# Kernel optimization log

Measured on AMD Instinct MI355X. Metric: run time of the kernel, lower is better.

The kernel has to match this reference:

```python
import jax, jax.numpy as jnp
import numpy as np

B = 64        # decode batch (num_tokens)
S = 2048      # max_kv_len
H = 2048      # hidden_size
HQ = 16       # num query heads
HKV = 4       # num kv heads
D = 128       # head_dim
RD = 64       # rope_dim = head_dim * 0.5
P = B * S     # kv pool size
EPS = 1e-6
SCALE = D ** -0.5


def rms_norm(x, w):
    xf = x.astype(jnp.float32)
    var = jnp.mean(xf * xf, axis=-1, keepdims=True)
    return (w.astype(jnp.float32) * (xf * jax.lax.rsqrt(var + EPS))).astype(x.dtype)


def rotate_half(x):
    x1, x2 = x[..., : x.shape[-1] // 2], x[..., x.shape[-1] // 2:]
    return jnp.concatenate([-x2, x1], axis=-1)


def apply_rope(x, cos, sin):
    # x: [T, heads, D]; cos/sin: [T, 1, RD]; partial rotary on first RD dims
    x_rot, x_pass = x[..., :RD], x[..., RD:]
    x_emb = x_rot * cos + rotate_half(x_rot) * sin
    return jnp.concatenate([x_emb, x_pass], axis=-1)


def setup_inputs() -> dict:
    key = jax.random.key(0)
    ks = jax.random.split(key, 10)
    f32 = jnp.float32
    hidden_states = jax.random.normal(ks[0], (B, H), f32)
    Wq = jax.random.normal(ks[1], (HQ * D, H), f32) * 0.02
    Wk = jax.random.normal(ks[2], (HKV * D, H), f32) * 0.02
    Wv = jax.random.normal(ks[3], (HKV * D, H), f32) * 0.02
    Wo = jax.random.normal(ks[4], (H, HQ * D), f32) * 0.02
    q_norm_w = jnp.ones((D,), f32)
    k_norm_w = jnp.ones((D,), f32)
    key_cache = jax.random.normal(ks[5], (P, HKV, D), f32)
    value_cache = jax.random.normal(ks[6], (P, HKV, D), f32)
    seq_lens = jax.random.randint(ks[7], (B,), S // 2, S + 1).astype(jnp.int32)
    req_pool_indices = jnp.arange(B, dtype=jnp.int32)
    req_to_token = jnp.arange(P, dtype=jnp.int32).reshape(B, S)
    out_cache_loc = (req_pool_indices * S + (seq_lens - 1)).astype(jnp.int32)
    # RoPE tables for the current decode positions (seq_len - 1)
    pos = (seq_lens - 1).astype(f32)
    inv_freq = 1.0 / (10000.0 ** (jnp.arange(0, RD, 2, dtype=f32) / RD))  # [RD/2]
    ang = pos[:, None] * inv_freq[None, :]                                 # [B, RD/2]
    cos = jnp.concatenate([jnp.cos(ang), jnp.cos(ang)], axis=-1)           # [B, RD]
    sin = jnp.concatenate([jnp.sin(ang), jnp.sin(ang)], axis=-1)
    return dict(hidden_states=hidden_states, Wq=Wq, Wk=Wk, Wv=Wv,
                q_norm_w=q_norm_w, k_norm_w=k_norm_w, Wo=Wo,
                key_cache=key_cache, value_cache=value_cache, cos=cos, sin=sin,
                req_to_token=req_to_token, req_pool_indices=req_pool_indices,
                seq_lens=seq_lens, out_cache_loc=out_cache_loc)


def reference(hidden_states, Wq, Wk, Wv, q_norm_w, k_norm_w, Wo,
              key_cache, value_cache, cos, sin,
              req_to_token, req_pool_indices, seq_lens, out_cache_loc):
    G = HQ // HKV  # GQA groups
    # fused qkv projection
    q = (hidden_states @ Wq.T).reshape(B, HQ, D)
    k = (hidden_states @ Wk.T).reshape(B, HKV, D)
    v = (hidden_states @ Wv.T).reshape(B, HKV, D)
    # per-head RMSNorm
    q = rms_norm(q, q_norm_w)
    k = rms_norm(k, k_norm_w)
    # partial rotary embedding (sliding_attention layer -> rope applied)
    q = apply_rope(q, cos[:, None, :], sin[:, None, :])
    k = apply_rope(k, cos[:, None, :], sin[:, None, :])
    # write new token K/V into the paged pool
    key_cache = key_cache.at[out_cache_loc].set(k)
    value_cache = value_cache.at[out_cache_loc].set(v)
    # paged gather: [B, S, HKV, D]
    token_indices = req_to_token[req_pool_indices]
    k_pad = key_cache[token_indices].transpose(0, 2, 1, 3)    # [B, HKV, S, D]
    v_pad = value_cache[token_indices].transpose(0, 2, 1, 3)  # [B, HKV, S, D]
    # padding mask over kv positions
    mask = jnp.arange(S)[None, :] < seq_lens[:, None]          # [B, S]
    # attention (q_len = 1 per request), grouped-query
    qg = q.reshape(B, HKV, G, D)
    scores = jnp.einsum('bkgd,bksd->bkgs', qg, k_pad) * SCALE  # [B, HKV, G, S]
    scores = jnp.where(mask[:, None, None, :], scores, jnp.finfo(scores.dtype).min)
    attn = jax.nn.softmax(scores, axis=-1)
    out = jnp.einsum('bkgs,bksd->bkgd', attn, v_pad).reshape(B, HQ * D)
    return out @ Wo.T
```

## Files before the change

kernel.cpp:

```cpp
#include <hip/hip_runtime.h>
#include <math.h>

#define BB 64
#define SS 2048
#define HH 2048
#define HQ 16
#define HKV 4
#define DD 128
#define RD 64
#define GG 4
#define QKV_N 3072
#define SCALE 0.08838834764831845f
#define KSPLIT 16
#define KRANGE (HH / KSPLIT)
#define NSPLIT 8
#define CHUNK 256

__device__ __forceinline__ void gemm_tile(const float* __restrict__ A,
                                          const float* __restrict__ W,
                                          float* __restrict__ Cpart,
                                          int ldC, int colbase, int wrow0, int ks) {
  __shared__ __align__(16) float As[32][68];
  __shared__ __align__(16) float Ws[32][132];
  const int tid = threadIdx.x;
  const int tm = tid >> 4, tn = tid & 15;
  float acc[4][8] = {};
  const int k0 = ks * KRANGE;
  for (int kk = k0; kk < k0 + KRANGE; kk += 32) {
    #pragma unroll
    for (int p = tid; p < 512; p += 256) {
      const int mm = p >> 3, cc = p & 7;
      const float4 a = *(const float4*)(A + (size_t)mm * HH + kk + cc * 4);
      As[cc*4+0][mm] = a.x; As[cc*4+1][mm] = a.y;
      As[cc*4+2][mm] = a.z; As[cc*4+3][mm] = a.w;
    }
    #pragma unroll
    for (int p = tid; p < 1024; p += 256) {
      const int rr = p >> 3, cc = p & 7;
      const float4 w = *(const float4*)(W + (size_t)(wrow0 + rr) * HH + kk + cc * 4);
      Ws[cc*4+0][rr] = w.x; Ws[cc*4+1][rr] = w.y;
      Ws[cc*4+2][rr] = w.z; Ws[cc*4+3][rr] = w.w;
    }
    __syncthreads();
    #pragma unroll
    for (int k = 0; k < 32; k++) {
      const float4 av  = *(const float4*)&As[k][tm * 4];
      const float4 wv0 = *(const float4*)&Ws[k][tn * 8];
      const float4 wv1 = *(const float4*)&Ws[k][tn * 8 + 4];
      const float a4[4] = {av.x, av.y, av.z, av.w};
      const float w8[8] = {wv0.x, wv0.y, wv0.z, wv0.w, wv1.x, wv1.y, wv1.z, wv1.w};
      #pragma unroll
      for (int i = 0; i < 4; i++)
        #pragma unroll
        for (int j = 0; j < 8; j++)
          acc[i][j] += a4[i] * w8[j];
    }
    __syncthreads();
  }
  #pragma unroll
  for (int i = 0; i < 4; i++) {
    float* dst = Cpart + (size_t)(tm*4 + i) * ldC + colbase + tn*8;
    *(float4*)dst       = make_float4(acc[i][0], acc[i][1], acc[i][2], acc[i][3]);
    *(float4*)(dst + 4) = make_float4(acc[i][4], acc[i][5], acc[i][6], acc[i][7]);
  }
}

__global__ __launch_bounds__(256) void maple_gemm_qkv(const float* __restrict__ A,
                                                      const float* __restrict__ Wq,
                                                      const float* __restrict__ Wk,
                                                      const float* __restrict__ Wv,
                                                      float* __restrict__ qkv_part) {
  const int col0 = blockIdx.x * 128;
  const int ks = blockIdx.y;
  const float* W; int wrow0;
  if (col0 < 2048)      { W = Wq; wrow0 = col0; }
  else if (col0 < 2560) { W = Wk; wrow0 = col0 - 2048; }
  else                  { W = Wv; wrow0 = col0 - 2560; }
  gemm_tile(A, W, qkv_part + (size_t)ks * BB * QKV_N, QKV_N, col0, wrow0, ks);
}

__global__ __launch_bounds__(256) void maple_gemm_o(const float* __restrict__ A,
                                                    const float* __restrict__ W,
                                                    float* __restrict__ out_part) {
  const int col0 = blockIdx.x * 128;
  const int ks = blockIdx.y;
  gemm_tile(A, W, out_part + (size_t)ks * BB * HH, HH, col0, col0, ks);
}

__global__ __launch_bounds__(128) void maple_norm_rope(const float* __restrict__ qkv_part,
                                                       const float* __restrict__ qw,
                                                       const float* __restrict__ kw,
                                                       const float* __restrict__ cosb,
                                                       const float* __restrict__ sinb,
                                                       float* __restrict__ qbuf,
                                                       float* __restrict__ kbuf,
                                                       float* __restrict__ vbuf) {
  const int h = blockIdx.x;
  const int b = blockIdx.y;
  const int tid = threadIdx.x;
  __shared__ float xs[128];
  __shared__ float red[2];
  int col; const float* w;
  if (h < HQ) { col = h * DD + tid;                w = qw; }
  else        { col = 2048 + (h - HQ) * DD + tid;  w = kw; }
  float x = 0.0f;
  #pragma unroll
  for (int ks = 0; ks < KSPLIT; ks++)
    x += qkv_part[(size_t)ks * BB * QKV_N + (size_t)b * QKV_N + col];
  if (h >= HQ) {
    float xv = 0.0f;
    #pragma unroll
    for (int ks = 0; ks < KSPLIT; ks++)
      xv += qkv_part[(size_t)ks * BB * QKV_N + (size_t)b * QKV_N + 2560 + (h - HQ) * DD + tid];
    vbuf[((size_t)b * HKV + (h - HQ)) * DD + tid] = xv;
  }
  float ss = x * x;
  #pragma unroll
  for (int off = 1; off < 64; off <<= 1) ss += __shfl_xor(ss, off);
  if ((tid & 63) == 0) red[tid >> 6] = ss;
  __syncthreads();
  const float var = (red[0] + red[1]) * (1.0f / 128.0f);
  const float r = rsqrtf(var + 1e-6f);
  const float xn = w[tid] * x * r;
  xs[tid] = xn;
  __syncthreads();
  float o;
  if (tid < 32)      o = xn * cosb[b*RD + tid] - xs[tid + 32] * sinb[b*RD + tid];
  else if (tid < 64) o = xn * cosb[b*RD + tid] + xs[tid - 32] * sinb[b*RD + tid];
  else               o = xn;
  if (h < HQ) qbuf[((size_t)b * HQ  + h)        * DD + tid] = o;
  else        kbuf[((size_t)b * HKV + (h - HQ)) * DD + tid] = o;
}

__global__ __launch_bounds__(256) void maple_attn_split(const float* __restrict__ qbuf,
                                                        const float* __restrict__ kbuf,
                                                        const float* __restrict__ vbuf,
                                                        const float* __restrict__ kc,
                                                        const float* __restrict__ vc,
                                                        const int* __restrict__ req_to_token,
                                                        const int* __restrict__ rpi,
                                                        const int* __restrict__ seq_lens,
                                                        float* __restrict__ part,
                                                        float* __restrict__ part_l) {
  const int c  = blockIdx.x;
  const int kh = blockIdx.y;
  const int b  = blockIdx.z;
  const int tid = threadIdx.x;
  const int w = tid >> 6, lane = tid & 63, tsub = lane >> 4, dsub = lane & 15;
  const int L  = seq_lens[b];
  const int last = L - 1;
  const int s0 = c * CHUNK;
  const int s1 = min(s0 + CHUNK, L);

  __shared__ float qs[GG * DD];
  for (int i = tid; i < GG * DD; i += 256)
    qs[i] = qbuf[((size_t)b * HQ + kh * GG) * DD + i] * SCALE;
  __syncthreads();

  float qf[GG][8];
  #pragma unroll
  for (int g = 0; g < GG; g++)
    #pragma unroll
    for (int j = 0; j < 8; j++) qf[g][j] = qs[g * DD + dsub * 8 + j];

  float l[GG] = {0,0,0,0}, acc[GG][8] = {};
  const int* trow = req_to_token + (size_t)rpi[b] * SS;
  const size_t fresh = ((size_t)b * HKV + kh) * DD + dsub * 8;

  for (int s = s0 + w * 4; s < s1; s += 16) {
    const int t = s + tsub;
    const bool valid = (t < s1);
    const int tt = valid ? t : s0;
    float4 k0, k1, v0, v1;
    if (tt == last) {
      k0 = *(const float4*)(kbuf + fresh); k1 = *(const float4*)(kbuf + fresh + 4);
      v0 = *(const float4*)(vbuf + fresh); v1 = *(const float4*)(vbuf + fresh + 4);
    } else {
      const int ci = trow[tt];
      const size_t base = ((size_t)ci * HKV + kh) * DD + dsub * 8;
      k0 = *(const float4*)(kc + base); k1 = *(const float4*)(kc + base + 4);
      v0 = *(const float4*)(vc + base); v1 = *(const float4*)(vc + base + 4);
    }
    float sc[GG];
    #pragma unroll
    for (int g = 0; g < GG; g++) {
      sc[g] = qf[g][0]*k0.x + qf[g][1]*k0.y + qf[g][2]*k0.z + qf[g][3]*k0.w
            + qf[g][4]*k1.x + qf[g][5]*k1.y + qf[g][6]*k1.z + qf[g][7]*k1.w;
    }
    #pragma unroll
    for (int off = 1; off < 16; off <<= 1) {
      #pragma unroll
      for (int g = 0; g < GG; g++) sc[g] += __shfl_xor(sc[g], off);
    }
    #pragma unroll
    for (int g = 0; g < GG; g++) {
      const float p = valid ? __expf(sc[g]) : 0.0f;
      l[g] += p;
      acc[g][0] += p*v0.x; acc[g][1] += p*v0.y; acc[g][2] += p*v0.z; acc[g][3] += p*v0.w;
      acc[g][4] += p*v1.x; acc[g][5] += p*v1.y; acc[g][6] += p*v1.z; acc[g][7] += p*v1.w;
    }
  }

  #pragma unroll
  for (int g = 0; g < GG; g++) {
    l[g] += __shfl_xor(l[g], 16);
    l[g] += __shfl_xor(l[g], 32);
    #pragma unroll
    for (int j = 0; j < 8; j++) {
      acc[g][j] += __shfl_xor(acc[g][j], 16);
      acc[g][j] += __shfl_xor(acc[g][j], 32);
    }
  }

  __shared__ float wacc[4][GG][DD];
  __shared__ float wl[4][GG];
  if (lane < 16) {
    #pragma unroll
    for (int g = 0; g < GG; g++)
      #pragma unroll
      for (int j = 0; j < 8; j++) wacc[w][g][lane * 8 + j] = acc[g][j];
  }
  if (lane == 0) {
    #pragma unroll
    for (int g = 0; g < GG; g++) wl[w][g] = l[g];
  }
  __syncthreads();

  const size_t pbase = ((size_t)b * HKV + kh) * NSPLIT + c;
  for (int i = tid; i < GG * DD; i += 256) {
    const int g = i >> 7, d = i & 127;
    part[pbase * (GG * DD) + i] =
        wacc[0][g][d] + wacc[1][g][d] + wacc[2][g][d] + wacc[3][g][d];
  }
  if (tid < GG)
    part_l[pbase * GG + tid] = wl[0][tid] + wl[1][tid] + wl[2][tid] + wl[3][tid];
}

__global__ __launch_bounds__(256) void maple_attn_combine(const float* __restrict__ part,
                                                          const float* __restrict__ part_l,
                                                          float* __restrict__ attn_out) {
  const int kh = blockIdx.x;
  const int b  = blockIdx.y;
  const int tid = threadIdx.x;
  const size_t pb = ((size_t)b * HKV + kh) * NSPLIT;
  for (int i = tid; i < GG * DD; i += 256) {
    const int g = i >> 7, d = i & 127;
    float o = 0.0f, Ls = 0.0f;
    #pragma unroll
    for (int c = 0; c < NSPLIT; c++) {
      o  += part[(pb + c) * (GG * DD) + i];
      Ls += part_l[(pb + c) * GG + g];
    }
    attn_out[((size_t)b * HQ + kh * GG + g) * DD + d] = o / Ls;
  }
}

__global__ __launch_bounds__(256) void maple_reduce_out(const float* __restrict__ out_part,
                                                        float* __restrict__ out) {
  const int i = blockIdx.x * 256 + threadIdx.x;
  float s = 0.0f;
  #pragma unroll
  for (int ks = 0; ks < KSPLIT; ks++)
    s += out_part[(size_t)ks * (BB * HH) + i];
  out[i] = s;
}

extern "C" void kernel_launch(void* const* d_in, const int* in_sizes, int n_in,
                              void* d_out, int out_size, void* d_ws, size_t ws_size,
                              hipStream_t stream) {
  const float* hidden = (const float*)d_in[0];
  const float* Wq     = (const float*)d_in[1];
  const float* Wk     = (const float*)d_in[2];
  const float* Wv     = (const float*)d_in[3];
  const float* qnw    = (const float*)d_in[4];
  const float* knw    = (const float*)d_in[5];
  const float* Wo     = (const float*)d_in[6];
  const float* key_cache   = (const float*)d_in[7];
  const float* value_cache = (const float*)d_in[8];
  const float* cosb   = (const float*)d_in[9];
  const float* sinb   = (const float*)d_in[10];
  const int* req_to_token = (const int*)d_in[11];
  const int* rpi          = (const int*)d_in[12];
  const int* seq_lens     = (const int*)d_in[13];
  float* out = (float*)d_out;

  float* ws = (float*)d_ws;
  float* qkv_part = ws;
  float* out_part = qkv_part + 3145728;
  float* qbuf     = out_part + 2097152;
  float* kbuf     = qbuf + 131072;
  float* vbuf     = kbuf + 32768;
  float* attn_out = vbuf + 32768;
  float* part     = attn_out + 131072;
  float* part_l   = part + 1048576;

  maple_gemm_qkv<<<dim3(24, KSPLIT), 256, 0, stream>>>(hidden, Wq, Wk, Wv, qkv_part);
  maple_norm_rope<<<dim3(HQ + HKV, BB), 128, 0, stream>>>(qkv_part, qnw, knw, cosb, sinb,
                                                          qbuf, kbuf, vbuf);
  maple_attn_split<<<dim3(NSPLIT, HKV, BB), 256, 0, stream>>>(qbuf, kbuf, vbuf,
                                                              key_cache, value_cache,
                                                              req_to_token, rpi, seq_lens,
                                                              part, part_l);
  maple_attn_combine<<<dim3(HKV, BB), 256, 0, stream>>>(part, part_l, attn_out);
  maple_gemm_o<<<dim3(16, KSPLIT), 256, 0, stream>>>(attn_out, Wo, out_part);
  maple_reduce_out<<<dim3(512), 256, 0, stream>>>(out_part, out);
}
```

Before: 596.1 us.

## Prefetch GEMM tiles into registers, halve QKV k-split, skip empty attention chunks

The shared GEMM tile loop now loads the next K-slice of A and W into registers while computing on the current shared-memory tile, so global-load latency can overlap with FMAs. The QKV projection k-split drops from 16 to 8, which halves the partial-sum traffic written by the GEMM and read back by norm_rope, but also halves the number of blocks. Attention split blocks whose chunk starts past the sequence length now exit early, and combine only sums the chunks that were written. The prefetch adds register pressure, and the smaller QKV grid may underfill the GPU.

Measured after the change: 583.3 us. 1.02x faster.

```diff
diff --git a/kernel.cpp b/kernel.cpp
--- a/kernel.cpp
+++ b/kernel.cpp
@@ -11,37 +11,61 @@
 #define GG 4
 #define QKV_N 3072
 #define SCALE 0.08838834764831845f
-#define KSPLIT 16
-#define KRANGE (HH / KSPLIT)
+#define QKSPLIT 8
+#define OSPLIT 16
 #define NSPLIT 8
 #define CHUNK 256
 
 __device__ __forceinline__ void gemm_tile(const float* __restrict__ A,
                                           const float* __restrict__ W,
                                           float* __restrict__ Cpart,
-                                          int ldC, int colbase, int wrow0, int ks) {
+                                          int ldC, int colbase, int wrow0,
+                                          int k0, int krange) {
   __shared__ __align__(16) float As[32][68];
   __shared__ __align__(16) float Ws[32][132];
   const int tid = threadIdx.x;
   const int tm = tid >> 4, tn = tid & 15;
   float acc[4][8] = {};
-  const int k0 = ks * KRANGE;
-  for (int kk = k0; kk < k0 + KRANGE; kk += 32) {
-    #pragma unroll
-    for (int p = tid; p < 512; p += 256) {
-      const int mm = p >> 3, cc = p & 7;
-      const float4 a = *(const float4*)(A + (size_t)mm * HH + kk + cc * 4);
-      As[cc*4+0][mm] = a.x; As[cc*4+1][mm] = a.y;
-      As[cc*4+2][mm] = a.z; As[cc*4+3][mm] = a.w;
-    }
-    #pragma unroll
-    for (int p = tid; p < 1024; p += 256) {
-      const int rr = p >> 3, cc = p & 7;
-      const float4 w = *(const float4*)(W + (size_t)(wrow0 + rr) * HH + kk + cc * 4);
-      Ws[cc*4+0][rr] = w.x; Ws[cc*4+1][rr] = w.y;
-      Ws[cc*4+2][rr] = w.z; Ws[cc*4+3][rr] = w.w;
+  const int kend = k0 + krange;
+
+  float4 areg[2], wreg[4];
+  #pragma unroll
+  for (int q = 0; q < 2; q++) {
+    const int p = tid + q * 256, mm = p >> 3, cc = p & 7;
+    areg[q] = *(const float4*)(A + (size_t)mm * HH + k0 + cc * 4);
+  }
+  #pragma unroll
+  for (int q = 0; q < 4; q++) {
+    const int p = tid + q * 256, rr = p >> 3, cc = p & 7;
+    wreg[q] = *(const float4*)(W + (size_t)(wrow0 + rr) * HH + k0 + cc * 4);
+  }
+
+  for (int kk = k0; kk < kend; kk += 32) {
+    #pragma unroll
+    for (int q = 0; q < 2; q++) {
+      const int p = tid + q * 256, mm = p >> 3, cc = p & 7;
+      As[cc*4+0][mm] = areg[q].x; As[cc*4+1][mm] = areg[q].y;
+      As[cc*4+2][mm] = areg[q].z; As[cc*4+3][mm] = areg[q].w;
+    }
+    #pragma unroll
+    for (int q = 0; q < 4; q++) {
+      const int p = tid + q * 256, rr = p >> 3, cc = p & 7;
+      Ws[cc*4+0][rr] = wreg[q].x; Ws[cc*4+1][rr] = wreg[q].y;
+      Ws[cc*4+2][rr] = wreg[q].z; Ws[cc*4+3][rr] = wreg[q].w;
     }
     __syncthreads();
+    if (kk + 32 < kend) {
+      #pragma unroll
+      for (int q = 0; q < 2; q++) {
+        const int p = tid + q * 256, mm = p >> 3, cc = p & 7;
+        areg[q] = *(const float4*)(A + (size_t)mm * HH + kk + 32 + cc * 4);
+      }
+      #pragma unroll
+      for (int q = 0; q < 4; q++) {
+        const int p = tid + q * 256, rr = p >> 3, cc = p & 7;
+        wreg[q] = *(const float4*)(W + (size_t)(wrow0 + rr) * HH + kk + 32 + cc * 4);
+      }
+    }
     #pragma unroll
     for (int k = 0; k < 32; k++) {
       const float4 av  = *(const float4*)&As[k][tm * 4];
@@ -76,7 +100,8 @@
   if (col0 < 2048)      { W = Wq; wrow0 = col0; }
   else if (col0 < 2560) { W = Wk; wrow0 = col0 - 2048; }
   else                  { W = Wv; wrow0 = col0 - 2560; }
-  gemm_tile(A, W, qkv_part + (size_t)ks * BB * QKV_N, QKV_N, col0, wrow0, ks);
+  gemm_tile(A, W, qkv_part + (size_t)ks * BB * QKV_N, QKV_N, col0, wrow0,
+            ks * (HH / QKSPLIT), HH / QKSPLIT);
 }
 
 __global__ __launch_bounds__(256) void maple_gemm_o(const float* __restrict__ A,
@@ -84,7 +109,8 @@
                                                     float* __restrict__ out_part) {
   const int col0 = blockIdx.x * 128;
   const int ks = blockIdx.y;
-  gemm_tile(A, W, out_part + (size_t)ks * BB * HH, HH, col0, col0, ks);
+  gemm_tile(A, W, out_part + (size_t)ks * BB * HH, HH, col0, col0,
+            ks * (HH / OSPLIT), HH / OSPLIT);
 }
 
 __global__ __launch_bounds__(128) void maple_norm_rope(const float* __restrict__ qkv_part,
@@ -105,12 +131,12 @@
   else        { col = 2048 + (h - HQ) * DD + tid;  w = kw; }
   float x = 0.0f;
   #pragma unroll
-  for (int ks = 0; ks < KSPLIT; ks++)
+  for (int ks = 0; ks < QKSPLIT; ks++)
     x += qkv_part[(size_t)ks * BB * QKV_N + (size_t)b * QKV_N + col];
   if (h >= HQ) {
     float xv = 0.0f;
     #pragma unroll
-    for (int ks = 0; ks < KSPLIT; ks++)
+    for (int ks = 0; ks < QKSPLIT; ks++)
       xv += qkv_part[(size_t)ks * BB * QKV_N + (size_t)b * QKV_N + 2560 + (h - HQ) * DD + tid];
     vbuf[((size_t)b * HKV + (h - HQ)) * DD + tid] = xv;
   }
@@ -145,11 +171,12 @@
   const int c  = blockIdx.x;
   const int kh = blockIdx.y;
   const int b  = blockIdx.z;
+  const int L  = seq_lens[b];
+  const int s0 = c * CHUNK;
+  if (s0 >= L) return;
   const int tid = threadIdx.x;
   const int w = tid >> 6, lane = tid & 63, tsub = lane >> 4, dsub = lane & 15;
-  const int L  = seq_lens[b];
   const int last = L - 1;
-  const int s0 = c * CHUNK;
   const int s1 = min(s0 + CHUNK, L);
 
   __shared__ float qs[GG * DD];
@@ -238,16 +265,17 @@
 
 __global__ __launch_bounds__(256) void maple_attn_combine(const float* __restrict__ part,
                                                           const float* __restrict__ part_l,
+                                                          const int* __restrict__ seq_lens,
                                                           float* __restrict__ attn_out) {
   const int kh = blockIdx.x;
   const int b  = blockIdx.y;
   const int tid = threadIdx.x;
+  const int nc = (seq_lens[b] + CHUNK - 1) / CHUNK;
   const size_t pb = ((size_t)b * HKV + kh) * NSPLIT;
   for (int i = tid; i < GG * DD; i += 256) {
     const int g = i >> 7, d = i & 127;
     float o = 0.0f, Ls = 0.0f;
-    #pragma unroll
-    for (int c = 0; c < NSPLIT; c++) {
+    for (int c = 0; c < nc; c++) {
       o  += part[(pb + c) * (GG * DD) + i];
       Ls += part_l[(pb + c) * GG + g];
     }
@@ -260,7 +288,7 @@
   const int i = blockIdx.x * 256 + threadIdx.x;
   float s = 0.0f;
   #pragma unroll
-  for (int ks = 0; ks < KSPLIT; ks++)
+  for (int ks = 0; ks < OSPLIT; ks++)
     s += out_part[(size_t)ks * (BB * HH) + i];
   out[i] = s;
 }
@@ -286,7 +314,7 @@
 
   float* ws = (float*)d_ws;
   float* qkv_part = ws;
-  float* out_part = qkv_part + 3145728;
+  float* out_part = qkv_part + 1572864;
   float* qbuf     = out_part + 2097152;
   float* kbuf     = qbuf + 131072;
   float* vbuf     = kbuf + 32768;
@@ -294,14 +322,14 @@
   float* part     = attn_out + 131072;
   float* part_l   = part + 1048576;
 
-  maple_gemm_qkv<<<dim3(24, KSPLIT), 256, 0, stream>>>(hidden, Wq, Wk, Wv, qkv_part);
+  maple_gemm_qkv<<<dim3(24, QKSPLIT), 256, 0, stream>>>(hidden, Wq, Wk, Wv, qkv_part);
   maple_norm_rope<<<dim3(HQ + HKV, BB), 128, 0, stream>>>(qkv_part, qnw, knw, cosb, sinb,
                                                           qbuf, kbuf, vbuf);
   maple_attn_split<<<dim3(NSPLIT, HKV, BB), 256, 0, stream>>>(qbuf, kbuf, vbuf,
                                                               key_cache, value_cache,
                                                               req_to_token, rpi, seq_lens,
                                                               part, part_l);
-  maple_attn_combine<<<dim3(HKV, BB), 256, 0, stream>>>(part, part_l, attn_out);
-  maple_gemm_o<<<dim3(16, KSPLIT), 256, 0, stream>>>(attn_out, Wo, out_part);
+  maple_attn_combine<<<dim3(HKV, BB), 256, 0, stream>>>(part, part_l, seq_lens, attn_out);
+  maple_gemm_o<<<dim3(16, OSPLIT), 256, 0, stream>>>(attn_out, Wo, out_part);
   maple_reduce_out<<<dim3(512), 256, 0, stream>>>(out_part, out);
 }
```
